# Performance work log

Measured on AMD Instinct MI355X. Metric: run time of the kernel, lower is better.

Reference implementation:

```python
import jax, jax.numpy as jnp
import numpy as np

T, B, E, H, V, L = 128, 64, 1024, 1024, 10000, 2


def setup_inputs() -> dict:
    key = jax.random.key(0)
    ks = jax.random.split(key, 10)
    k = 1.0 / np.sqrt(H)
    u = lambda kk, shape, a: jax.random.uniform(kk, shape, jnp.float32, -a, a)
    return {
        "emb_table": u(ks[0], (V, E), 0.1),
        "W_in0": u(ks[1], (H, E), k),   # first layer input weight (no bias in linear_W)
        "Wh0": u(ks[2], (H, H), k),
        "b0": u(ks[3], (H,), k),
        "W_in1": u(ks[4], (H, H), k),
        "Wh1": u(ks[5], (H, H), k),
        "b1": u(ks[6], (H,), k),
        "Wdec": u(ks[7], (V, H), 0.1),
        "bdec": jnp.zeros((V,), jnp.float32),
        "hidden": jnp.zeros((L, B, H), jnp.float32),
        "tokens": jax.random.randint(ks[8], (T, B), 0, V, jnp.int32),
    }


def reference(emb_table, W_in0, Wh0, b0, W_in1, Wh1, b1, Wdec, bdec, hidden, tokens):
    # dp_keep_prob = 1.0 -> dropout is identity
    x_emb = emb_table[tokens]  # [T, B, E]

    def step(h, x):
        # h: [L, B, H]; x: [B, E]
        h0 = jnp.tanh(x @ W_in0.T + h[0] @ Wh0.T + b0)
        h1 = jnp.tanh(h0 @ W_in1.T + h[1] @ Wh1.T + b1)
        logits_t = h1 @ Wdec.T + bdec  # [B, V]
        return jnp.stack([h0, h1]), logits_t

    h_final, logits = jax.lax.scan(step, hidden, x_emb)
    return logits, h_final  # [T, B, V], [L, B, H]
```

## Files before the change

kernel.cpp:

```cpp
#include <hip/hip_runtime.h>
#include <hip/hip_bf16.h>
#include <stdint.h>

typedef __bf16 bf16_t;
typedef __bf16 bf16x8 __attribute__((ext_vector_type(8)));
typedef __bf16 bf16x4 __attribute__((ext_vector_type(4)));
typedef float  floatx4 __attribute__((ext_vector_type(4)));

#define T_STEPS 128
#define BATCH   64
#define EDIM    1024
#define HDIM    1024
#define VOCAB   10000
#define MROWS   (T_STEPS * BATCH)
#define RNN_BLOCKS 128
#define DEC_BLOCKS 128
#define BH      (BATCH * HDIM)
#define FSTRIDE 16
#define XF_OFF  (128 * FSTRIDE)
#define OUT0    ((size_t)MROWS * VOCAB)

__device__ __forceinline__ floatx4 mfma16(bf16x8 a, bf16x8 b, floatx4 c) {
    return __builtin_amdgcn_mfma_f32_16x16x32_bf16(a, b, c, 0, 0, 0);
}

__device__ __forceinline__ void gl_lds16(const bf16_t* g, bf16_t* l) {
    __builtin_amdgcn_global_load_lds(
        (const __attribute__((address_space(1))) void*)g,
        (__attribute__((address_space(3))) void*)l, 16, 0, 0);
}

__device__ __forceinline__ void store_bf16_bypass(bf16_t* p, float v) {
    union { bf16_t b; unsigned short u; } cv;
    cv.b = (bf16_t)v;
    unsigned int d = cv.u;
    asm volatile("global_store_short %0, %1, off sc0 sc1"
                 :: "v"(p), "v"(d) : "memory");
}

__device__ __forceinline__ void wait_flag1(const int* p) {
    while (__hip_atomic_load(p, __ATOMIC_RELAXED, __HIP_MEMORY_SCOPE_AGENT) == 0)
        __builtin_amdgcn_s_sleep(1);
}


__global__ void setup_kernel(const float* __restrict__ emb,
                             const float* __restrict__ W_in0, const float* __restrict__ Wh0,
                             const float* __restrict__ W_in1, const float* __restrict__ Wh1,
                             const float* __restrict__ Wdec,
                             const float* __restrict__ hidden, const int* __restrict__ tok,
                             bf16_t* __restrict__ Xemb,
                             bf16_t* __restrict__ Win0b, bf16_t* __restrict__ Wh0b,
                             bf16_t* __restrict__ Win1b, bf16_t* __restrict__ Wh1b,
                             bf16_t* __restrict__ Wdecb,
                             bf16_t* __restrict__ h0all, bf16_t* __restrict__ h1all,
                             int* __restrict__ flags) {
    const int b = blockIdx.x, tid = threadIdx.x;
    if (b < 4096) {
        const int which = b >> 10;
        const float* s = which == 0 ? W_in0 : which == 1 ? Wh0 : which == 2 ? W_in1 : Wh1;
        bf16_t*      d = which == 0 ? Win0b : which == 1 ? Wh0b : which == 2 ? Win1b : Wh1b;
        int i = ((b & 1023) * 256 + tid) * 4;
        float4 v = *(const float4*)(s + i);
        bf16x4 o; o.x = (bf16_t)v.x; o.y = (bf16_t)v.y; o.z = (bf16_t)v.z; o.w = (bf16_t)v.w;
        *(bf16x4*)(d + i) = o;
    } else if (b < 14096) {
        int i = ((b - 4096) * 256 + tid) * 4;
        float4 v = *(const float4*)(Wdec + i);
        bf16x4 o; o.x = (bf16_t)v.x; o.y = (bf16_t)v.y; o.z = (bf16_t)v.z; o.w = (bf16_t)v.w;
        *(bf16x4*)(Wdecb + i) = o;
    } else if (b < 22288) {
        int row = b - 14096;
        int t = tok[row];
        int e = tid * 4;
        float4 v = *(const float4*)(emb + (size_t)t * EDIM + e);
        bf16x4 o; o.x = (bf16_t)v.x; o.y = (bf16_t)v.y; o.z = (bf16_t)v.z; o.w = (bf16_t)v.w;
        *(bf16x4*)(Xemb + (size_t)row * EDIM + e) = o;
    } else {
        int i = ((b - 22288) * 256 + tid) * 4;
        float4 v0 = *(const float4*)(hidden + i);
        float4 v1 = *(const float4*)(hidden + BH + i);
        bf16x4 o0, o1;
        o0.x = (bf16_t)v0.x; o0.y = (bf16_t)v0.y; o0.z = (bf16_t)v0.z; o0.w = (bf16_t)v0.w;
        o1.x = (bf16_t)v1.x; o1.y = (bf16_t)v1.y; o1.z = (bf16_t)v1.z; o1.w = (bf16_t)v1.w;
        *(bf16x4*)(h0all + i) = o0;
        *(bf16x4*)(h1all + i) = o1;
        if (b == 22288)
            for (int j = tid; j < XF_OFF + 512; j += 256) flags[j] = 0;
    }
}


__global__ __launch_bounds__(256, 1) void fused_kernel(
    bf16_t* __restrict__ X0,
    const bf16_t* __restrict__ Xemb,
    const bf16_t* __restrict__ Win0b,
    const float*  __restrict__ b0,
    const bf16_t* __restrict__ Wh0b,
    const bf16_t* __restrict__ Win1b,
    const bf16_t* __restrict__ Wh1b,
    const float*  __restrict__ b1,
    const bf16_t* __restrict__ Wdecb,
    const float*  __restrict__ bdec,
    float* __restrict__ out,
    bf16_t* __restrict__ h0all,
    bf16_t* __restrict__ h1all,
    int* __restrict__ flags)
{
    __shared__ __align__(16) char smem[65536];
    const int tid  = threadIdx.x;
    const int lane = tid & 63;
    const int wave = tid >> 6;
    const int quad = lane >> 4;
    const int l16  = lane & 15;
    int* f0 = flags;
    int* f1 = flags + 64 * FSTRIDE;
    int* xf = flags + XF_OFF;
    const floatx4 fzero = {0.f, 0.f, 0.f, 0.f};

    if (blockIdx.x >= RNN_BLOCKS) {
        const int d  = blockIdx.x - RNN_BLOCKS;
        const int wm = wave & 1;
        const int wn = wave >> 1;
        bf16_t* sA = (bf16_t*)smem;
        bf16_t* sW = (bf16_t*)(smem + 8192);

        for (int u = d; u < 512; u += DEC_BLOCKS) {
            const int mTile = (u >> 3) * 128;
            const int nTile = (u & 7) * 128;
            floatx4 acc[4][4];
            #pragma unroll
            for (int i = 0; i < 4; ++i)
                #pragma unroll
                for (int j = 0; j < 4; ++j) acc[i][j] = fzero;
            for (int kk = 0; kk < EDIM; kk += 32) {
                __syncthreads();
                #pragma unroll
                for (int j = 0; j < 2; ++j) {
                    int c   = tid + j * 256;
                    int row = c >> 2;
                    int sub = c & 3;
                    gl_lds16(Xemb  + (size_t)(mTile + row) * EDIM + kk + sub * 8, sA + c * 8);
                    gl_lds16(Win0b + (size_t)(nTile + row) * EDIM + kk + sub * 8, sW + c * 8);
                }
                __syncthreads();
                bf16x8 af[4], wf[4];
                #pragma unroll
                for (int mi = 0; mi < 4; ++mi)
                    af[mi] = *(const bf16x8*)(sA + (wm * 64 + mi * 16 + l16) * 32 + quad * 8);
                #pragma unroll
                for (int ni = 0; ni < 4; ++ni)
                    wf[ni] = *(const bf16x8*)(sW + (wn * 64 + ni * 16 + l16) * 32 + quad * 8);
                #pragma unroll
                for (int mi = 0; mi < 4; ++mi)
                    #pragma unroll
                    for (int ni = 0; ni < 4; ++ni)
                        acc[mi][ni] = mfma16(af[mi], wf[ni], acc[mi][ni]);
            }
            #pragma unroll
            for (int ni = 0; ni < 4; ++ni) {
                int col = nTile + wn * 64 + ni * 16 + l16;
                float bv = b0[col];
                #pragma unroll
                for (int mi = 0; mi < 4; ++mi) {
                    #pragma unroll
                    for (int r = 0; r < 4; ++r) {
                        int row = mTile + wm * 64 + mi * 16 + quad * 4 + r;
                        store_bf16_bypass(X0 + (size_t)row * HDIM + col,
                                          acc[mi][ni][r] + bv);
                    }
                }
            }
            asm volatile("s_waitcnt vmcnt(0)" ::: "memory");
            __syncthreads();
            if (tid == 0)
                __hip_atomic_store(&xf[u], 1, __ATOMIC_RELAXED, __HIP_MEMORY_SCOPE_AGENT);
            __syncthreads();
        }

        int vt, tp0, tpN;
        if (d < 79) { vt = d;      tp0 = 0;  tpN = (d < 49) ? 32 : 64; }
        else        { vt = d - 79; tp0 = 32; tpN = 64; }
        const bf16_t* Adec = h1all + BH;
        const int nTile = vt * 128;
        int vc = 0;
        for (int tp = tp0; tp < tpN; ++tp) {
            const int need = 2 * tp + 2;
            if (wave == 0) {
                while (!__all(vc >= need)) {
                    if (vc < need) {
                        vc = __hip_atomic_load(&f1[lane * FSTRIDE], __ATOMIC_RELAXED,
                                               __HIP_MEMORY_SCOPE_AGENT);
                        if (vc < need) __builtin_amdgcn_s_sleep(32);
                    }
                }
            }
            __syncthreads();
            const int mTile = tp * 128;
            floatx4 acc[4][4];
            #pragma unroll
            for (int i = 0; i < 4; ++i)
                #pragma unroll
                for (int j = 0; j < 4; ++j) acc[i][j] = fzero;
            for (int kk = 0; kk < HDIM; kk += 32) {
                __syncthreads();
                #pragma unroll
                for (int j = 0; j < 2; ++j) {
                    int c   = tid + j * 256;
                    int row = c >> 2;
                    int sub = c & 3;
                    gl_lds16(Adec + (size_t)(mTile + row) * HDIM + kk + sub * 8, sA + c * 8);
                    int wrow = nTile + row;
                    if (wrow >= VOCAB) wrow = VOCAB - 1;
                    gl_lds16(Wdecb + (size_t)wrow * HDIM + kk + sub * 8, sW + c * 8);
                }
                __syncthreads();
                bf16x8 af[4], wf[4];
                #pragma unroll
                for (int mi = 0; mi < 4; ++mi)
                    af[mi] = *(const bf16x8*)(sA + (wm * 64 + mi * 16 + l16) * 32 + quad * 8);
                #pragma unroll
                for (int ni = 0; ni < 4; ++ni)
                    wf[ni] = *(const bf16x8*)(sW + (wn * 64 + ni * 16 + l16) * 32 + quad * 8);
                #pragma unroll
                for (int mi = 0; mi < 4; ++mi)
                    #pragma unroll
                    for (int ni = 0; ni < 4; ++ni)
                        acc[mi][ni] = mfma16(af[mi], wf[ni], acc[mi][ni]);
            }
            #pragma unroll
            for (int ni = 0; ni < 4; ++ni) {
                int col = nTile + wn * 64 + ni * 16 + l16;
                if (col < VOCAB) {
                    float bv = bdec[col];
                    #pragma unroll
                    for (int mi = 0; mi < 4; ++mi) {
                        #pragma unroll
                        for (int r = 0; r < 4; ++r) {
                            int row = mTile + wm * 64 + mi * 16 + quad * 4 + r;
                            out[(size_t)row * VOCAB + col] = acc[mi][ni][r] + bv;
                        }
                    }
                }
            }
            __syncthreads();
        }
        return;
    }

    const bool isL1 = blockIdx.x >= 64;
    const int cb    = blockIdx.x & 63;
    const int cbase = cb * 16;
    const int colg  = cbase + l16;
    const int arow  = (wave * 16 + l16) * HDIM;
    const int orow0 = wave * 16 + quad * 4;

    {
        const bf16_t* W0 = isL1 ? Win1b : Wh0b;
        for (int c = tid; c < 2048; c += 256) {
            int kc2 = c >> 6, ln = c & 63;
            const bf16_t* src = W0 + (size_t)(cbase + (ln & 15)) * HDIM + kc2 * 32 + (ln >> 4) * 8;
            *(int4*)(smem + c * 16) = *(const int4*)src;
        }
        if (isL1) {
            for (int c = tid; c < 2048; c += 256) {
                int kc2 = c >> 6, ln = c & 63;
                const bf16_t* src = Wh1b + (size_t)(cbase + (ln & 15)) * HDIM + kc2 * 32 + (ln >> 4) * 8;
                *(int4*)(smem + 32768 + c * 16) = *(const int4*)src;
            }
        }
    }
    __syncthreads();

    if (!isL1) {
        const int nt0 = cb >> 3;
        wait_flag1(&xf[nt0]);
        float xr[4];
        #pragma unroll
        for (int r = 0; r < 4; ++r)
            xr[r] = (float)X0[(size_t)(orow0 + r) * HDIM + colg];
        int xdone = 0;
        int vc = 0;
        for (int t = 0; t < T_STEPS; ++t) {
            if (t > 0) {
                if (wave == 0) {
                    while (!__all(vc >= t)) {
                        if (vc < t) {
                            vc = __hip_atomic_load(&f0[lane * FSTRIDE], __ATOMIC_RELAXED,
                                                   __HIP_MEMORY_SCOPE_AGENT);
                            if (vc < t) __builtin_amdgcn_s_sleep(1);
                        }
                    }
                }
                __syncthreads();
            }
            const bf16_t* Ap = h0all + (size_t)t * BH;
            bf16x8 av[32];
            #pragma unroll
            for (int kc = 0; kc < 32; ++kc)
                av[kc] = *(const bf16x8*)(Ap + arow + kc * 32 + quad * 8);
            float xn[4];
            if (t + 1 < T_STEPS) {
                int m = (t + 1) >> 1;
                if (m > xdone) { wait_flag1(&xf[m * 8 + nt0]); xdone = m; }
                #pragma unroll
                for (int r = 0; r < 4; ++r)
                    xn[r] = (float)X0[((size_t)(t + 1) * BATCH + orow0 + r) * HDIM + colg];
            }
            __builtin_amdgcn_sched_barrier(0);
            floatx4 a0 = fzero, a1 = fzero;
            #pragma unroll
            for (int kc = 0; kc < 32; ++kc) {
                bf16x8 wv = *(const bf16x8*)(smem + kc * 1024 + lane * 16);
                if (kc & 1) a1 = mfma16(av[kc], wv, a1);
                else        a0 = mfma16(av[kc], wv, a0);
            }
            bf16_t* dst = h0all + (size_t)(t + 1) * BH;
            #pragma unroll
            for (int r = 0; r < 4; ++r) {
                float hv = tanhf(xr[r] + a0[r] + a1[r]);
                store_bf16_bypass(dst + (size_t)(orow0 + r) * HDIM + colg, hv);
                if (t == T_STEPS - 1)
                    out[OUT0 + (size_t)(orow0 + r) * HDIM + colg] = hv;
            }
            if (t + 1 < T_STEPS) {
                #pragma unroll
                for (int r = 0; r < 4; ++r) xr[r] = xn[r];
            }
            asm volatile("s_waitcnt vmcnt(0)" ::: "memory");
            __syncthreads();
            if (tid == 0)
                __hip_atomic_store(&f0[cb * FSTRIDE], t + 1, __ATOMIC_RELAXED,
                                   __HIP_MEMORY_SCOPE_AGENT);
        }
    } else {
        const float bb = b1[colg];
        int vc0 = 0, vc1 = 0;
        for (int t = 0; t < T_STEPS; ++t) {
            if (wave == 0) {
                while (!__all(vc0 >= t + 1)) {
                    if (vc0 < t + 1) {
                        vc0 = __hip_atomic_load(&f0[lane * FSTRIDE], __ATOMIC_RELAXED,
                                                __HIP_MEMORY_SCOPE_AGENT);
                        if (vc0 < t + 1) __builtin_amdgcn_s_sleep(1);
                    }
                }
            }
            __syncthreads();
            const bf16_t* A0 = h0all + (size_t)(t + 1) * BH;
            bf16x8 av0[32];
            #pragma unroll
            for (int kc = 0; kc < 32; ++kc)
                av0[kc] = *(const bf16x8*)(A0 + arow + kc * 32 + quad * 8);
            __builtin_amdgcn_sched_barrier(0);
            floatx4 aA = fzero, aB = fzero;
            #pragma unroll
            for (int kc = 0; kc < 32; ++kc) {
                bf16x8 wv1 = *(const bf16x8*)(smem + kc * 1024 + lane * 16);
                if (kc & 1) aB = mfma16(av0[kc], wv1, aB);
                else        aA = mfma16(av0[kc], wv1, aA);
            }
            if (t > 0) {
                if (wave == 0) {
                    while (!__all(vc1 >= t)) {
                        if (vc1 < t) {
                            vc1 = __hip_atomic_load(&f1[lane * FSTRIDE], __ATOMIC_RELAXED,
                                                    __HIP_MEMORY_SCOPE_AGENT);
                            if (vc1 < t) __builtin_amdgcn_s_sleep(1);
                        }
                    }
                }
                __syncthreads();
            }
            const bf16_t* A1 = h1all + (size_t)t * BH;
            bf16x8 av1[32];
            #pragma unroll
            for (int kc = 0; kc < 32; ++kc)
                av1[kc] = *(const bf16x8*)(A1 + arow + kc * 32 + quad * 8);
            __builtin_amdgcn_sched_barrier(0);
            #pragma unroll
            for (int kc = 0; kc < 32; ++kc) {
                bf16x8 wv2 = *(const bf16x8*)(smem + 32768 + kc * 1024 + lane * 16);
                if (kc & 1) aB = mfma16(av1[kc], wv2, aB);
                else        aA = mfma16(av1[kc], wv2, aA);
            }
            bf16_t* dst = h1all + (size_t)(t + 1) * BH;
            #pragma unroll
            for (int r = 0; r < 4; ++r) {
                float hv = tanhf(aA[r] + aB[r] + bb);
                store_bf16_bypass(dst + (size_t)(orow0 + r) * HDIM + colg, hv);
                if (t == T_STEPS - 1)
                    out[OUT0 + BH + (size_t)(orow0 + r) * HDIM + colg] = hv;
            }
            asm volatile("s_waitcnt vmcnt(0)" ::: "memory");
            __syncthreads();
            if (tid == 0)
                __hip_atomic_store(&f1[cb * FSTRIDE], t + 1, __ATOMIC_RELAXED,
                                   __HIP_MEMORY_SCOPE_AGENT);
        }
    }
}


extern "C" void kernel_launch(void* const* d_in, const int* in_sizes, int n_in,
                              void* d_out, int out_size, void* d_ws, size_t ws_size,
                              hipStream_t stream) {
    (void)in_sizes; (void)n_in; (void)out_size; (void)ws_size;
    const float* emb    = (const float*)d_in[0];
    const float* W_in0  = (const float*)d_in[1];
    const float* Wh0    = (const float*)d_in[2];
    const float* b0     = (const float*)d_in[3];
    const float* W_in1  = (const float*)d_in[4];
    const float* Wh1    = (const float*)d_in[5];
    const float* b1     = (const float*)d_in[6];
    const float* Wdec   = (const float*)d_in[7];
    const float* bdec   = (const float*)d_in[8];
    const float* hidden = (const float*)d_in[9];
    const int*   tokens = (const int*)d_in[10];
    float* out = (float*)d_out;

    char* ws = (char*)d_ws;
    auto alloc = [&](size_t bytes) {
        char* p = ws; ws += (bytes + 255) & ~(size_t)255; return p;
    };
    bf16_t* Xemb  = (bf16_t*)alloc((size_t)MROWS * EDIM * 2);
    bf16_t* X0    = (bf16_t*)alloc((size_t)MROWS * HDIM * 2);
    bf16_t* Win0b = (bf16_t*)alloc((size_t)HDIM * EDIM * 2);
    bf16_t* Wh0b  = (bf16_t*)alloc((size_t)HDIM * HDIM * 2);
    bf16_t* Win1b = (bf16_t*)alloc((size_t)HDIM * HDIM * 2);
    bf16_t* Wh1b  = (bf16_t*)alloc((size_t)HDIM * HDIM * 2);
    bf16_t* Wdecb = (bf16_t*)alloc((size_t)VOCAB * HDIM * 2);
    bf16_t* h1all = (bf16_t*)alloc((size_t)(T_STEPS + 1) * BATCH * HDIM * 2);
    bf16_t* h0all = (bf16_t*)alloc((size_t)(T_STEPS + 1) * BATCH * HDIM * 2);
    int*    flags = (int*)alloc((XF_OFF + 512) * 4);

    setup_kernel<<<dim3(22352), 256, 0, stream>>>(
        emb, W_in0, Wh0, W_in1, Wh1, Wdec, hidden, tokens,
        Xemb, Win0b, Wh0b, Win1b, Wh1b, Wdecb, h0all, h1all, flags);

    fused_kernel<<<dim3(RNN_BLOCKS + DEC_BLOCKS), 256, 0, stream>>>(
        X0, Xemb, Win0b, b0, Wh0b, Win1b, Wh1b, b1, Wdecb, bdec,
        out, h0all, h1all, flags);
}
```

Measured before the change: 1.645 ms.

## Stream recurrent activations through per-wave LDS ring with global_load_lds

Replaces the bulk register preload of 32 activation fragments per step with a 16-slot per-wave LDS ring filled by global_load_lds, using staged vmcnt waits so MFMAs start as soon as the first fragments land. Layer-1 blocks now wait for both the layer-0 and layer-1 flags in one merged poll and run a single fused 64-fragment loop, and layer-0 folds the embedding-projection flag check into its per-step poll. Decoder output stores become nontemporal. This is meant to cut register pressure and load-to-compute latency on the serial recurrence critical path. In exchange it doubles shared memory to 128KB and adds ordering hazards: a ring slot is refilled right after it is read, and the raw vmcnt counts must match the loads the compiler actually emits.

```diff
diff --git a/kernel.cpp b/kernel.cpp
--- a/kernel.cpp
+++ b/kernel.cpp
@@ -36,11 +36,6 @@
     unsigned int d = cv.u;
     asm volatile("global_store_short %0, %1, off sc0 sc1"
                  :: "v"(p), "v"(d) : "memory");
-}
-
-__device__ __forceinline__ void wait_flag1(const int* p) {
-    while (__hip_atomic_load(p, __ATOMIC_RELAXED, __HIP_MEMORY_SCOPE_AGENT) == 0)
-        __builtin_amdgcn_s_sleep(1);
 }
 
 
@@ -107,7 +102,7 @@
     bf16_t* __restrict__ h1all,
     int* __restrict__ flags)
 {
-    __shared__ __align__(16) char smem[65536];
+    __shared__ __align__(16) char smem[131072];
     const int tid  = threadIdx.x;
     const int lane = tid & 63;
     const int wave = tid >> 6;
@@ -238,7 +233,8 @@
                         #pragma unroll
                         for (int r = 0; r < 4; ++r) {
                             int row = mTile + wm * 64 + mi * 16 + quad * 4 + r;
-                            out[(size_t)row * VOCAB + col] = acc[mi][ni][r] + bv;
+                            __builtin_nontemporal_store(acc[mi][ni][r] + bv,
+                                                        &out[(size_t)row * VOCAB + col]);
                         }
                     }
                 }
@@ -252,7 +248,7 @@
     const int cb    = blockIdx.x & 63;
     const int cbase = cb * 16;
     const int colg  = cbase + l16;
-    const int arow  = (wave * 16 + l16) * HDIM;
+    const int alane = (wave * 16 + l16) * HDIM + quad * 8;
     const int orow0 = wave * 16 + quad * 4;
 
     {
@@ -274,46 +270,60 @@
 
     if (!isL1) {
         const int nt0 = cb >> 3;
-        wait_flag1(&xf[nt0]);
+        if (wave == 0 && lane == 0)
+            while (__hip_atomic_load(&xf[nt0], __ATOMIC_RELAXED,
+                                     __HIP_MEMORY_SCOPE_AGENT) == 0)
+                __builtin_amdgcn_s_sleep(2);
+        __syncthreads();
         float xr[4];
         #pragma unroll
         for (int r = 0; r < 4; ++r)
             xr[r] = (float)X0[(size_t)(orow0 + r) * HDIM + colg];
-        int xdone = 0;
+        char* ring = smem + 32768 + wave * 16384;
         int vc = 0;
         for (int t = 0; t < T_STEPS; ++t) {
             if (t > 0) {
                 if (wave == 0) {
-                    while (!__all(vc >= t)) {
-                        if (vc < t) {
+                    int m = (t + 1) >> 1; if (m > 63) m = 63;
+                    const int xfi = m * 8 + nt0;
+                    int xv = 0;
+                    for (;;) {
+                        if (vc < t)
                             vc = __hip_atomic_load(&f0[lane * FSTRIDE], __ATOMIC_RELAXED,
                                                    __HIP_MEMORY_SCOPE_AGENT);
-                            if (vc < t) __builtin_amdgcn_s_sleep(1);
-                        }
+                        if (lane == 0 && xv == 0)
+                            xv = __hip_atomic_load(&xf[xfi], __ATOMIC_RELAXED,
+                                                   __HIP_MEMORY_SCOPE_AGENT);
+                        if (__all(vc >= t) && __all(lane != 0 || xv != 0)) break;
+                        __builtin_amdgcn_s_sleep(1);
                     }
                 }
                 __syncthreads();
             }
             const bf16_t* Ap = h0all + (size_t)t * BH;
-            bf16x8 av[32];
-            #pragma unroll
-            for (int kc = 0; kc < 32; ++kc)
-                av[kc] = *(const bf16x8*)(Ap + arow + kc * 32 + quad * 8);
             float xn[4];
             if (t + 1 < T_STEPS) {
-                int m = (t + 1) >> 1;
-                if (m > xdone) { wait_flag1(&xf[m * 8 + nt0]); xdone = m; }
                 #pragma unroll
                 for (int r = 0; r < 4; ++r)
                     xn[r] = (float)X0[((size_t)(t + 1) * BATCH + orow0 + r) * HDIM + colg];
             }
-            __builtin_amdgcn_sched_barrier(0);
+            #pragma unroll
+            for (int i = 0; i < 16; ++i)
+                gl_lds16(Ap + alane + i * 32, (bf16_t*)(ring + i * 1024));
             floatx4 a0 = fzero, a1 = fzero;
             #pragma unroll
             for (int kc = 0; kc < 32; ++kc) {
+                if (kc < 16)      asm volatile("s_waitcnt vmcnt(15)" ::: "memory");
+                else if (kc < 20) asm volatile("s_waitcnt vmcnt(12)" ::: "memory");
+                else if (kc < 24) asm volatile("s_waitcnt vmcnt(8)"  ::: "memory");
+                else if (kc < 28) asm volatile("s_waitcnt vmcnt(4)"  ::: "memory");
+                else              asm volatile("s_waitcnt vmcnt(0)"  ::: "memory");
+                bf16x8 av = *(const bf16x8*)(ring + (kc & 15) * 1024 + lane * 16);
+                if (kc < 16)
+                    gl_lds16(Ap + alane + (kc + 16) * 32, (bf16_t*)(ring + (kc & 15) * 1024));
                 bf16x8 wv = *(const bf16x8*)(smem + kc * 1024 + lane * 16);
-                if (kc & 1) a1 = mfma16(av[kc], wv, a1);
-                else        a0 = mfma16(av[kc], wv, a0);
+                if (kc & 1) a1 = mfma16(av, wv, a1);
+                else        a0 = mfma16(av, wv, a0);
             }
             bf16_t* dst = h0all + (size_t)(t + 1) * BH;
             #pragma unroll
@@ -335,54 +345,45 @@
         }
     } else {
         const float bb = b1[colg];
+        char* ring = smem + 65536 + wave * 16384;
         int vc0 = 0, vc1 = 0;
         for (int t = 0; t < T_STEPS; ++t) {
             if (wave == 0) {
-                while (!__all(vc0 >= t + 1)) {
-                    if (vc0 < t + 1) {
+                while (!(__all(vc0 >= t + 1) && __all(vc1 >= t))) {
+                    if (vc0 < t + 1)
                         vc0 = __hip_atomic_load(&f0[lane * FSTRIDE], __ATOMIC_RELAXED,
                                                 __HIP_MEMORY_SCOPE_AGENT);
-                        if (vc0 < t + 1) __builtin_amdgcn_s_sleep(1);
-                    }
+                    if (vc1 < t)
+                        vc1 = __hip_atomic_load(&f1[lane * FSTRIDE], __ATOMIC_RELAXED,
+                                                __HIP_MEMORY_SCOPE_AGENT);
+                    __builtin_amdgcn_s_sleep(1);
                 }
             }
             __syncthreads();
             const bf16_t* A0 = h0all + (size_t)(t + 1) * BH;
-            bf16x8 av0[32];
-            #pragma unroll
-            for (int kc = 0; kc < 32; ++kc)
-                av0[kc] = *(const bf16x8*)(A0 + arow + kc * 32 + quad * 8);
-            __builtin_amdgcn_sched_barrier(0);
+            const bf16_t* A1 = h1all + (size_t)t * BH;
+            #pragma unroll
+            for (int i = 0; i < 16; ++i)
+                gl_lds16(A0 + alane + i * 32, (bf16_t*)(ring + i * 1024));
             floatx4 aA = fzero, aB = fzero;
             #pragma unroll
-            for (int kc = 0; kc < 32; ++kc) {
-                bf16x8 wv1 = *(const bf16x8*)(smem + kc * 1024 + lane * 16);
-                if (kc & 1) aB = mfma16(av0[kc], wv1, aB);
-                else        aA = mfma16(av0[kc], wv1, aA);
-            }
-            if (t > 0) {
-                if (wave == 0) {
-                    while (!__all(vc1 >= t)) {
-                        if (vc1 < t) {
-                            vc1 = __hip_atomic_load(&f1[lane * FSTRIDE], __ATOMIC_RELAXED,
-                                                    __HIP_MEMORY_SCOPE_AGENT);
-                            if (vc1 < t) __builtin_amdgcn_s_sleep(1);
-                        }
-                    }
-                }
-                __syncthreads();
-            }
-            const bf16_t* A1 = h1all + (size_t)t * BH;
-            bf16x8 av1[32];
-            #pragma unroll
-            for (int kc = 0; kc < 32; ++kc)
-                av1[kc] = *(const bf16x8*)(A1 + arow + kc * 32 + quad * 8);
-            __builtin_amdgcn_sched_barrier(0);
-            #pragma unroll
-            for (int kc = 0; kc < 32; ++kc) {
-                bf16x8 wv2 = *(const bf16x8*)(smem + 32768 + kc * 1024 + lane * 16);
-                if (kc & 1) aB = mfma16(av1[kc], wv2, aB);
-                else        aA = mfma16(av1[kc], wv2, aA);
+            for (int f = 0; f < 64; ++f) {
+                if (f < 48)       asm volatile("s_waitcnt vmcnt(15)" ::: "memory");
+                else if (f < 52)  asm volatile("s_waitcnt vmcnt(12)" ::: "memory");
+                else if (f < 56)  asm volatile("s_waitcnt vmcnt(8)"  ::: "memory");
+                else if (f < 60)  asm volatile("s_waitcnt vmcnt(4)"  ::: "memory");
+                else              asm volatile("s_waitcnt vmcnt(0)"  ::: "memory");
+                bf16x8 av = *(const bf16x8*)(ring + (f & 15) * 1024 + lane * 16);
+                if (f < 48) {
+                    const int nf = f + 16;
+                    const bf16_t* src = (nf < 32) ? (A0 + alane + nf * 32)
+                                                  : (A1 + alane + (nf - 32) * 32);
+                    gl_lds16(src, (bf16_t*)(ring + (f & 15) * 1024));
+                }
+                const char* wbase = (f < 32) ? (const char*)smem : (const char*)(smem + 32768);
+                bf16x8 wv = *(const bf16x8*)(wbase + (f & 31) * 1024 + lane * 16);
+                if (f & 1) aB = mfma16(av, wv, aB);
+                else       aA = mfma16(av, wv, aA);
             }
             bf16_t* dst = h1all + (size_t)(t + 1) * BH;
             #pragma unroll
```

Result: no change. 1.641 ms (-0.2%).
